# Optimization experiments

Hardware: AMD Instinct MI355X
Metric: run time of the kernel (lower is better)

Reference implementation:

```python
import jax, jax.numpy as jnp
import numpy as np

L, B, E, H, T, V = 256, 64, 256, 256, 16, 50000  # H = per-direction hidden; hidden_dim = 2H


def setup_inputs() -> dict:
    key = jax.random.key(0)
    ks = jax.random.split(key, 32)
    lengths = jnp.sort(jax.random.randint(ks[0], (B,), L // 2, L + 1))[::-1]  # descending, as pack_padded requires
    tokens = jax.random.randint(ks[1], (L, B), 1, V)
    valid = jnp.arange(L)[:, None] < lengths[None, :]
    tokens = jnp.where(valid, tokens, 0)  # pad_index = 0

    def gp(k, shape, s=0.1):
        return jax.random.normal(k, shape, dtype=jnp.float32) * s

    inp = {"tokens": tokens, "lengths": lengths, "emb": gp(ks[2], (V, E))}
    i = 3
    for layer, din in [(0, E), (1, 2 * H)]:
        for d in ("f", "b"):
            inp["w_ih_l%d%s" % (layer, d)] = gp(ks[i], (4 * H, din)); i += 1
            inp["w_hh_l%d%s" % (layer, d)] = gp(ks[i], (4 * H, H)); i += 1
            inp["b_ih_l%d%s" % (layer, d)] = gp(ks[i], (4 * H,)); i += 1
            inp["b_hh_l%d%s" % (layer, d)] = gp(ks[i], (4 * H,)); i += 1
    inp["w_out"] = gp(ks[i], (T, 2 * H)); i += 1
    inp["b_out"] = gp(ks[i], (T,)); i += 1
    inp["start_trans"] = gp(ks[i], (T,)); i += 1
    inp["end_trans"] = gp(ks[i], (T,)); i += 1
    inp["trans"] = gp(ks[i], (T, T))
    return inp


def lstm_layer(x, w_ih, w_hh, b_ih, b_hh):
    # x: [L, B, Din]; PyTorch gate order i, f, g, o; zero init state
    Hd = w_hh.shape[1]
    h0 = jnp.zeros((x.shape[1], Hd), x.dtype)

    def step(carry, xt):
        h, c = carry
        g = xt @ w_ih.T + b_ih + h @ w_hh.T + b_hh
        i, f, gg, o = jnp.split(g, 4, axis=-1)
        c = jax.nn.sigmoid(f) * c + jax.nn.sigmoid(i) * jnp.tanh(gg)
        h = jax.nn.sigmoid(o) * jnp.tanh(c)
        return (h, c), h

    _, ys = jax.lax.scan(step, (h0, h0), x)
    return ys  # [L, B, H]


def reverse_padded(x, lengths):
    # per-sequence time reversal over the first `length` steps (packed-sequence semantics)
    Ls = x.shape[0]
    t = jnp.arange(Ls)[:, None]
    idx = jnp.where(t < lengths[None, :], lengths[None, :] - 1 - t, t)  # [L, B]
    return jnp.take_along_axis(x, idx[:, :, None], axis=0)


def viterbi(emissions, mask, start_trans, end_trans, trans):
    # emissions [L, B, T], mask [L, B] bool -- pytorch-crf Viterbi decode, vectorized over batch
    score0 = start_trans[None, :] + emissions[0]  # [B, T]

    def step(score, inp):
        em_t, m_t = inp  # [B, T], [B]
        nxt = score[:, :, None] + trans[None, :, :] + em_t[:, None, :]  # [B, T, T]
        best = nxt.max(axis=1)
        idx = nxt.argmax(axis=1)  # index of previous tag
        score = jnp.where(m_t[:, None], best, score)  # freeze past end-of-sequence
        return score, idx

    score, hist = jax.lax.scan(step, score0, (emissions[1:], mask[1:]))  # hist [L-1, B, T]
    score = score + end_trans[None, :]
    best_score = score.max(axis=-1)
    last_tag = score.argmax(axis=-1)  # [B]

    def back(cur, inp):
        h_t, m_t = inp
        prev = jnp.take_along_axis(h_t, cur[:, None], axis=1)[:, 0]
        cur = jnp.where(m_t, prev, cur)
        return cur, cur

    _, tags_head = jax.lax.scan(back, last_tag, (hist, mask[1:]), reverse=True)  # [L-1, B]
    tags = jnp.concatenate([tags_head, last_tag[None, :]], axis=0)  # [L, B]
    tags = jnp.where(mask, tags, 0)
    return best_score, tags.astype(jnp.int32)


def reference(tokens, lengths, emb,
              w_ih_l0f, w_hh_l0f, b_ih_l0f, b_hh_l0f,
              w_ih_l0b, w_hh_l0b, b_ih_l0b, b_hh_l0b,
              w_ih_l1f, w_hh_l1f, b_ih_l1f, b_hh_l1f,
              w_ih_l1b, w_hh_l1b, b_ih_l1b, b_hh_l1b,
              w_out, b_out, start_trans, end_trans, trans):
    mask = tokens != 0  # pad_index = 0
    x = emb[tokens]  # [L, B, E]
    layers = [((w_ih_l0f, w_hh_l0f, b_ih_l0f, b_hh_l0f), (w_ih_l0b, w_hh_l0b, b_ih_l0b, b_hh_l0b)),
              ((w_ih_l1f, w_hh_l1f, b_ih_l1f, b_hh_l1f), (w_ih_l1b, w_hh_l1b, b_ih_l1b, b_hh_l1b))]
    for pf, pb in layers:
        fwd = lstm_layer(x, *pf)
        bwd = reverse_padded(lstm_layer(reverse_padded(x, lengths), *pb), lengths)
        x = jnp.concatenate([fwd, bwd], axis=-1) * mask[:, :, None]  # zero pads like pad_packed_sequence
    emissions = x @ w_out.T + b_out  # [L, B, T]
    best_score, tags = viterbi(emissions, mask, start_trans, end_trans, trans)
    return best_score, tags
```

## Files before the change

### kernel.cpp

```cpp
#include <hip/hip_runtime.h>
#include <hip/hip_bf16.h>
#include <math.h>

#define LSEQ 256
#define BB   64
#define EE   256
#define HH   256

__global__ __launch_bounds__(64)
void embed_kernel(const int* __restrict__ tokens, const float* __restrict__ emb,
                  float* __restrict__ x0) {
    int r = blockIdx.x;
    int tok = tokens[r];
    const float4* src = (const float4*)(emb + (size_t)tok * EE);
    float4* dst = (float4*)(x0 + (size_t)r * EE);
    dst[threadIdx.x] = src[threadIdx.x];
}

__global__ __launch_bounds__(256)
void pack_w3_kernel(const float* __restrict__ w0, const float* __restrict__ w1,
                    const float* __restrict__ w2, const float* __restrict__ w3,
                    float* __restrict__ W3) {
    __shared__ float t[16][65];
    const float* w = blockIdx.z == 0 ? w0 : blockIdx.z == 1 ? w1 : blockIdx.z == 2 ? w2 : w3;
    float* out = W3 + (size_t)blockIdx.z * 262144;
    int ut = blockIdx.y;
    int g = blockIdx.x >> 2, kt = blockIdx.x & 3;
    int k0 = kt * 64, tid = threadIdx.x;
    for (int e = tid; e < 1024; e += 256) {
        int ul = e >> 6, kl = e & 63;
        t[ul][kl] = w[(size_t)(g * 256 + ut * 16 + ul) * 256 + k0 + kl];
    }
    __syncthreads();
    for (int e = tid; e < 1024; e += 256) {
        int kl = e >> 4, ul = e & 15;
        out[(size_t)(ut * 256 + k0 + kl) * 64 + g * 16 + ul] = t[ul][kl];
    }
}

__global__ __launch_bounds__(256)
void init_cnt_kernel(int* __restrict__ cnt) {
    cnt[blockIdx.x * 256 + threadIdx.x] = 0;
}

__global__ __launch_bounds__(256)
void gemm_bias_kernel(const float* __restrict__ A, const float* __restrict__ W,
                      const float* __restrict__ b1, const float* __restrict__ b2,
                      float* __restrict__ C, int M, int N, int K) {
    const int BK = 16;
    __shared__ float As[BK][128];
    __shared__ float Bs[BK][128];
    int tid = threadIdx.x;
    int bm = blockIdx.x * 128;
    int bn = blockIdx.y * 128;
    int tm = (tid >> 4) << 3;
    int tn = (tid & 15) << 3;
    int lr = tid >> 1;
    int lc = (tid & 1) << 3;
    const float* Ap = A + (size_t)(bm + lr) * K + lc;
    const float* Wpt = W + (size_t)(bn + lr) * K + lc;
    float acc[8][8];
#pragma unroll
    for (int i = 0; i < 8; i++)
#pragma unroll
        for (int j = 0; j < 8; j++) acc[i][j] = 0.f;

    for (int k0 = 0; k0 < K; k0 += BK) {
        float4 a0 = *(const float4*)(Ap + k0);
        float4 a1 = *(const float4*)(Ap + k0 + 4);
        float4 w0 = *(const float4*)(Wpt + k0);
        float4 w1 = *(const float4*)(Wpt + k0 + 4);
        __syncthreads();
        As[lc+0][lr]=a0.x; As[lc+1][lr]=a0.y; As[lc+2][lr]=a0.z; As[lc+3][lr]=a0.w;
        As[lc+4][lr]=a1.x; As[lc+5][lr]=a1.y; As[lc+6][lr]=a1.z; As[lc+7][lr]=a1.w;
        Bs[lc+0][lr]=w0.x; Bs[lc+1][lr]=w0.y; Bs[lc+2][lr]=w0.z; Bs[lc+3][lr]=w0.w;
        Bs[lc+4][lr]=w1.x; Bs[lc+5][lr]=w1.y; Bs[lc+6][lr]=w1.z; Bs[lc+7][lr]=w1.w;
        __syncthreads();
#pragma unroll
        for (int k = 0; k < BK; k++) {
            float av[8], bv[8];
            *(float4*)&av[0] = *(const float4*)&As[k][tm];
            *(float4*)&av[4] = *(const float4*)&As[k][tm+4];
            *(float4*)&bv[0] = *(const float4*)&Bs[k][tn];
            *(float4*)&bv[4] = *(const float4*)&Bs[k][tn+4];
#pragma unroll
            for (int i = 0; i < 8; i++)
#pragma unroll
                for (int j = 0; j < 8; j++) acc[i][j] = fmaf(av[i], bv[j], acc[i][j]);
        }
    }
    float bj[8];
#pragma unroll
    for (int j = 0; j < 8; j++) bj[j] = b1[bn+tn+j] + b2[bn+tn+j];
#pragma unroll
    for (int i = 0; i < 8; i++) {
        float4 v0, v1;
        v0.x = acc[i][0]+bj[0]; v0.y = acc[i][1]+bj[1]; v0.z = acc[i][2]+bj[2]; v0.w = acc[i][3]+bj[3];
        v1.x = acc[i][4]+bj[4]; v1.y = acc[i][5]+bj[5]; v1.z = acc[i][6]+bj[6]; v1.w = acc[i][7]+bj[7];
        *(float4*)&C[(size_t)(bm+tm+i)*N + bn+tn]     = v0;
        *(float4*)&C[(size_t)(bm+tm+i)*N + bn+tn + 4] = v1;
    }
}

__global__ __launch_bounds__(256, 1)
void lstm_scan_kernel(const float* __restrict__ Gf, const float* __restrict__ Gb,
                      const float* __restrict__ W3f, const float* __restrict__ W3b,
                      const int* __restrict__ lengths, float* __restrict__ xout,
                      float* __restrict__ hg, int* __restrict__ cnt) {
    const int bid = blockIdx.x;
    const int dom = bid & 15;
    const int ut  = bid >> 4;
    const int dir = dom & 1;
    const int bt  = dom >> 1;
    const float* __restrict__ G = dir ? Gb : Gf;
    const float* __restrict__ W3 = (dir ? W3b : W3f) + (size_t)ut * 16384;
    float* hgD = hg + (size_t)dom * 4096;
    int* cntD = cnt + (size_t)dom * 8192;

    __shared__ float hs[2048];
    __shared__ float P[4096];
    __shared__ float lds_pad[16384];

    const int tid = threadIdx.x;
    const int kg = tid >> 5;
    const int cw = tid & 31;
    const int cb = (tid >> 4) & 7;
    const int cu = tid & 15;
    const int bg = bt * 8 + cb;
    const int ug = ut * 16 + cu;
    const int mylen = lengths[bg];

    float2 wreg[32];
#pragma unroll
    for (int kk = 0; kk < 32; kk++)
        wreg[kk] = *(const float2*)&W3[(size_t)(kg * 32 + kk) * 64 + cw * 2];

#pragma unroll
    for (int i = 0; i < 2; i++)
        *(float4*)&hs[(tid + 256 * i) * 4] = make_float4(0.f, 0.f, 0.f, 0.f);
    if (tid == 0 && mylen < 0) lds_pad[0] = 1.f;

    float cstate = 0.f;
    int tcur = dir ? (mylen - 1) : 0;
    const float* gr0 = G + ((size_t)tcur * BB + bg) * 1024 + ug;
    float gp0 = gr0[0], gp1 = gr0[256], gp2 = gr0[512], gp3 = gr0[768];
    __syncthreads();

    for (int s = 0; s < LSEQ; s++) {
        if (s > 0) {
            if (tid == 0) {
                const int* cp = &cntD[(s - 1) * 32];
                while (__hip_atomic_load(cp, __ATOMIC_RELAXED, __HIP_MEMORY_SCOPE_AGENT) < 16)
                    __builtin_amdgcn_s_sleep(1);
            }
            __syncthreads();
            const unsigned long long* src =
                (const unsigned long long*)(hgD + ((s - 1) & 1) * 2048);
            unsigned long long v[4];
#pragma unroll
            for (int i = 0; i < 4; i++)
                v[i] = __hip_atomic_load(src + tid + 256 * i, __ATOMIC_RELAXED,
                                         __HIP_MEMORY_SCOPE_AGENT);
#pragma unroll
            for (int i = 0; i < 4; i++)
                *(unsigned long long*)&hs[(tid + 256 * i) * 2] = v[i];
            __syncthreads();
        }

        float2 acc[8];
        const float4* h4 = (const float4*)hs;
#pragma unroll
        for (int b = 0; b < 8; b++) {
            float2 a = make_float2(0.f, 0.f);
            int hbase = b * 64 + kg * 8;
#pragma unroll
            for (int q = 0; q < 8; q++) {
                float4 hv = h4[hbase + q];
                a.x = fmaf(wreg[q*4+0].x, hv.x, a.x); a.y = fmaf(wreg[q*4+0].y, hv.x, a.y);
                a.x = fmaf(wreg[q*4+1].x, hv.y, a.x); a.y = fmaf(wreg[q*4+1].y, hv.y, a.y);
                a.x = fmaf(wreg[q*4+2].x, hv.z, a.x); a.y = fmaf(wreg[q*4+2].y, hv.z, a.y);
                a.x = fmaf(wreg[q*4+3].x, hv.w, a.x); a.y = fmaf(wreg[q*4+3].y, hv.w, a.y);
            }
            acc[b] = a;
        }
        const int wofs = (cw * 2) ^ (kg * 2);
#pragma unroll
        for (int b = 0; b < 8; b++)
            *(float2*)&P[kg * 512 + b * 64 + wofs] = acc[b];
        __syncthreads();

        float h = 0.f;
        if (tid < 128) {
            float g0 = gp0, g1 = gp1, g2 = gp2, g3 = gp3;
#pragma unroll
            for (int k2 = 0; k2 < 8; k2++) {
                int base = k2 * 512 + cb * 64;
                int x = k2 * 2;
                g0 += P[base + ((cu)      ^ x)];
                g1 += P[base + ((16 + cu) ^ x)];
                g2 += P[base + ((32 + cu) ^ x)];
                g3 += P[base + ((48 + cu) ^ x)];
            }
            float iv = 1.f / (1.f + expf(-g0));
            float fv = 1.f / (1.f + expf(-g1));
            float gv = tanhf(g2);
            float ov = 1.f / (1.f + expf(-g3));
            cstate = fv * cstate + iv * gv;
            h = ov * tanhf(cstate);
            atomicExch(&hgD[(s & 1) * 2048 + cb * 256 + ug], h);
        }
        asm volatile("s_waitcnt vmcnt(0)" ::: "memory");
        __syncthreads();
        if (tid == 0) atomicAdd(&cntD[s * 32], 1);

        if (tid < 128) {
            xout[(size_t)(tcur * BB + bg) * 512 + dir * 256 + ug] = (s < mylen) ? h : 0.f;
            if (s < 255) {
                int s2 = s + 1;
                tcur = dir ? (s2 < mylen ? mylen - 1 - s2 : s2) : s2;
                const float* gr = G + ((size_t)tcur * BB + bg) * 1024 + ug;
                gp0 = gr[0]; gp1 = gr[256]; gp2 = gr[512]; gp3 = gr[768];
            }
        }
    }
}

__global__ __launch_bounds__(256)
void emis_kernel(const float* __restrict__ x, const float* __restrict__ w_out,
                 const float* __restrict__ b_out, float* __restrict__ em) {
    __shared__ float ws_[16][516];
    __shared__ float xs[16][516];
    int tid = threadIdx.x;
    size_t r0 = (size_t)blockIdx.x * 16;
    for (int i4 = tid; i4 < 2048; i4 += 256) {
        int r = i4 >> 7, k4 = (i4 & 127) << 2;
        *(float4*)&ws_[r][k4] = *(const float4*)&w_out[r*512 + k4];
        *(float4*)&xs[r][k4]  = *(const float4*)&x[(r0 + r)*512 + k4];
    }
    __syncthreads();
    int rr = tid >> 4, n = tid & 15;
    const float4* xr = (const float4*)&xs[rr][0];
    const float4* wr = (const float4*)&ws_[n][0];
    float4 s; s.x = s.y = s.z = s.w = 0.f;
#pragma unroll 8
    for (int k = 0; k < 128; k++) {
        float4 a = xr[k], b = wr[k];
        s.x = fmaf(a.x,b.x,s.x); s.y = fmaf(a.y,b.y,s.y);
        s.z = fmaf(a.z,b.z,s.z); s.w = fmaf(a.w,b.w,s.w);
    }
    em[(r0+rr)*16 + n] = s.x+s.y+s.z+s.w + b_out[n];
}

__global__ __launch_bounds__(64)
void viterbi_kernel(const float* __restrict__ em, const int* __restrict__ tokens,
                    const float* __restrict__ start_trans, const float* __restrict__ end_trans,
                    const float* __restrict__ trans, float* __restrict__ out) {
    __shared__ float em_s[256][16];
    __shared__ float tr_s[16][16];
    __shared__ float sc[16];
    __shared__ unsigned char hist[255][16];
    int b = blockIdx.x, tid = threadIdx.x;
    for (int i = tid; i < 4096; i += 64) {
        int t = i >> 4, n = i & 15;
        em_s[t][n] = em[(size_t)t*1024 + b*16 + n];
    }
    for (int i = tid; i < 256; i += 64) ((float*)tr_s)[i] = trans[i];
    __syncthreads();
    if (tid < 16) sc[tid] = start_trans[tid] + em_s[0][tid];
    __syncthreads();
    for (int t = 1; t < 256; t++) {
        float best = 0.f; int arg = 0;
        if (tid < 16) {
            best = sc[0] + tr_s[0][tid];
#pragma unroll
            for (int i = 1; i < 16; i++) {
                float v = sc[i] + tr_s[i][tid];
                if (v > best) { best = v; arg = i; }
            }
            best += em_s[t][tid];
            hist[t-1][tid] = (unsigned char)arg;
        }
        bool m = tokens[t*64 + b] != 0;
        __syncthreads();
        if (tid < 16 && m) sc[tid] = best;
        __syncthreads();
    }
    if (tid == 0) {
        float best = sc[0] + end_trans[0]; int cur = 0;
        for (int jj = 1; jj < 16; jj++) {
            float v = sc[jj] + end_trans[jj];
            if (v > best) { best = v; cur = jj; }
        }
        out[b] = best;
        float* tags = out + 64;
        tags[255*64 + b] = (tokens[255*64+b] != 0) ? (float)cur : 0.f;
        for (int t = 254; t >= 0; t--) {
            if (tokens[(t+1)*64 + b] != 0) cur = hist[t][cur];
            tags[t*64 + b] = (tokens[t*64+b] != 0) ? (float)cur : 0.f;
        }
    }
}

extern "C" void kernel_launch(void* const* d_in, const int* in_sizes, int n_in,
                              void* d_out, int out_size, void* d_ws, size_t ws_size,
                              hipStream_t stream) {
    const int*   tokens   = (const int*)d_in[0];
    const int*   lengths  = (const int*)d_in[1];
    const float* emb      = (const float*)d_in[2];
    const float* w_ih_l0f = (const float*)d_in[3];
    const float* w_hh_l0f = (const float*)d_in[4];
    const float* b_ih_l0f = (const float*)d_in[5];
    const float* b_hh_l0f = (const float*)d_in[6];
    const float* w_ih_l0b = (const float*)d_in[7];
    const float* w_hh_l0b = (const float*)d_in[8];
    const float* b_ih_l0b = (const float*)d_in[9];
    const float* b_hh_l0b = (const float*)d_in[10];
    const float* w_ih_l1f = (const float*)d_in[11];
    const float* w_hh_l1f = (const float*)d_in[12];
    const float* b_ih_l1f = (const float*)d_in[13];
    const float* b_hh_l1f = (const float*)d_in[14];
    const float* w_ih_l1b = (const float*)d_in[15];
    const float* w_hh_l1b = (const float*)d_in[16];
    const float* b_ih_l1b = (const float*)d_in[17];
    const float* b_hh_l1b = (const float*)d_in[18];
    const float* w_out    = (const float*)d_in[19];
    const float* b_out    = (const float*)d_in[20];
    const float* start_tr = (const float*)d_in[21];
    const float* end_tr   = (const float*)d_in[22];
    const float* trans    = (const float*)d_in[23];

    float* ws  = (float*)d_ws;
    float* x0  = ws;
    float* x1  = x0 + 4194304;
    float* x2  = x1 + 8388608;
    float* Gf  = x2 + 8388608;
    float* Gb  = Gf + 16777216;
    float* W3  = Gb + 16777216;
    float* W3l0f = W3, *W3l0b = W3 + 262144, *W3l1f = W3 + 524288, *W3l1b = W3 + 786432;
    float* em  = x0;
    float* hg  = x0 + 1048576;
    int*   cnt = (int*)(x0 + 1179648);

    embed_kernel<<<16384, 64, 0, stream>>>(tokens, emb, x0);
    pack_w3_kernel<<<dim3(16, 16, 4), 256, 0, stream>>>(w_hh_l0f, w_hh_l0b, w_hh_l1f, w_hh_l1b, W3);

    dim3 gg(128, 8);
    gemm_bias_kernel<<<gg, 256, 0, stream>>>(x0, w_ih_l0f, b_ih_l0f, b_hh_l0f, Gf, 16384, 1024, 256);
    gemm_bias_kernel<<<gg, 256, 0, stream>>>(x0, w_ih_l0b, b_ih_l0b, b_hh_l0b, Gb, 16384, 1024, 256);
    init_cnt_kernel<<<1024, 256, 0, stream>>>(cnt);
    lstm_scan_kernel<<<256, 256, 0, stream>>>(Gf, Gb, W3l0f, W3l0b, lengths, x1, hg, cnt);

    gemm_bias_kernel<<<gg, 256, 0, stream>>>(x1, w_ih_l1f, b_ih_l1f, b_hh_l1f, Gf, 16384, 1024, 512);
    gemm_bias_kernel<<<gg, 256, 0, stream>>>(x1, w_ih_l1b, b_ih_l1b, b_hh_l1b, Gb, 16384, 1024, 512);
    lstm_scan_kernel<<<256, 256, 0, stream>>>(Gf, Gb, W3l1f, W3l1b, lengths, x2, hg, cnt + 131072);

    emis_kernel<<<1024, 256, 0, stream>>>(x2, w_out, b_out, em);
    viterbi_kernel<<<64, 64, 0, stream>>>(em, tokens, start_tr, end_tr, trans, (float*)d_out);
}
```

Measured before the change: 2.365 ms.

## Replace counter barrier with step-tagged hidden-state words in LSTM scan

Each hidden value is now published as a 64-bit word: the float in the low half and a step tag in the high half. Consumers spin directly on these words until every tag matches the expected step. This removes the per-step counter atomic, the single-thread spin, the memory-wait fence and one block barrier from the serial recurrence. It also drops the counter-reset kernel. In exchange the hidden-state buffer doubles in size, each thread polls eight words instead of reading four, and correctness now depends on stale tags in the reused workspace never matching the expected values.

```diff
diff --git a/kernel.cpp b/kernel.cpp
--- a/kernel.cpp
+++ b/kernel.cpp
@@ -36,11 +36,6 @@
         int kl = e >> 4, ul = e & 15;
         out[(size_t)(ut * 256 + k0 + kl) * 64 + g * 16 + ul] = t[ul][kl];
     }
-}
-
-__global__ __launch_bounds__(256)
-void init_cnt_kernel(int* __restrict__ cnt) {
-    cnt[blockIdx.x * 256 + threadIdx.x] = 0;
 }
 
 __global__ __launch_bounds__(256)
@@ -106,7 +101,7 @@
 void lstm_scan_kernel(const float* __restrict__ Gf, const float* __restrict__ Gb,
                       const float* __restrict__ W3f, const float* __restrict__ W3b,
                       const int* __restrict__ lengths, float* __restrict__ xout,
-                      float* __restrict__ hg, int* __restrict__ cnt) {
+                      unsigned long long* __restrict__ hg, int tagbase) {
     const int bid = blockIdx.x;
     const int dom = bid & 15;
     const int ut  = bid >> 4;
@@ -114,8 +109,7 @@
     const int bt  = dom >> 1;
     const float* __restrict__ G = dir ? Gb : Gf;
     const float* __restrict__ W3 = (dir ? W3b : W3f) + (size_t)ut * 16384;
-    float* hgD = hg + (size_t)dom * 4096;
-    int* cntD = cnt + (size_t)dom * 8192;
+    unsigned long long* hgD = hg + (size_t)dom * 4096;
 
     __shared__ float hs[2048];
     __shared__ float P[4096];
@@ -148,22 +142,27 @@
 
     for (int s = 0; s < LSEQ; s++) {
         if (s > 0) {
-            if (tid == 0) {
-                const int* cp = &cntD[(s - 1) * 32];
-                while (__hip_atomic_load(cp, __ATOMIC_RELAXED, __HIP_MEMORY_SCOPE_AGENT) < 16)
-                    __builtin_amdgcn_s_sleep(1);
-            }
-            __syncthreads();
-            const unsigned long long* src =
-                (const unsigned long long*)(hgD + ((s - 1) & 1) * 2048);
-            unsigned long long v[4];
-#pragma unroll
-            for (int i = 0; i < 4; i++)
+            const unsigned exp = (unsigned)(tagbase + s - 1);
+            const unsigned long long* src = hgD + ((s - 1) & 1) * 2048;
+            unsigned long long v[8];
+#pragma unroll
+            for (int i = 0; i < 8; i++)
                 v[i] = __hip_atomic_load(src + tid + 256 * i, __ATOMIC_RELAXED,
                                          __HIP_MEMORY_SCOPE_AGENT);
-#pragma unroll
-            for (int i = 0; i < 4; i++)
-                *(unsigned long long*)&hs[(tid + 256 * i) * 2] = v[i];
+            for (;;) {
+                bool ok = true;
+#pragma unroll
+                for (int i = 0; i < 8; i++) ok &= ((unsigned)(v[i] >> 32) == exp);
+                if (ok) break;
+#pragma unroll
+                for (int i = 0; i < 8; i++)
+                    if ((unsigned)(v[i] >> 32) != exp)
+                        v[i] = __hip_atomic_load(src + tid + 256 * i, __ATOMIC_RELAXED,
+                                                 __HIP_MEMORY_SCOPE_AGENT);
+            }
+#pragma unroll
+            for (int i = 0; i < 8; i++)
+                hs[tid + 256 * i] = __uint_as_float((unsigned)v[i]);
             __syncthreads();
         }
 
@@ -189,7 +188,6 @@
             *(float2*)&P[kg * 512 + b * 64 + wofs] = acc[b];
         __syncthreads();
 
-        float h = 0.f;
         if (tid < 128) {
             float g0 = gp0, g1 = gp1, g2 = gp2, g3 = gp3;
 #pragma unroll
@@ -206,14 +204,10 @@
             float gv = tanhf(g2);
             float ov = 1.f / (1.f + expf(-g3));
             cstate = fv * cstate + iv * gv;
-            h = ov * tanhf(cstate);
-            atomicExch(&hgD[(s & 1) * 2048 + cb * 256 + ug], h);
-        }
-        asm volatile("s_waitcnt vmcnt(0)" ::: "memory");
-        __syncthreads();
-        if (tid == 0) atomicAdd(&cntD[s * 32], 1);
-
-        if (tid < 128) {
+            float h = ov * tanhf(cstate);
+            unsigned long long pv =
+                ((unsigned long long)(unsigned)(tagbase + s) << 32) | __float_as_uint(h);
+            atomicExch(&hgD[(s & 1) * 2048 + cb * 256 + ug], pv);
             xout[(size_t)(tcur * BB + bg) * 512 + dir * 256 + ug] = (s < mylen) ? h : 0.f;
             if (s < 255) {
                 int s2 = s + 1;
@@ -338,8 +332,7 @@
     float* W3  = Gb + 16777216;
     float* W3l0f = W3, *W3l0b = W3 + 262144, *W3l1f = W3 + 524288, *W3l1b = W3 + 786432;
     float* em  = x0;
-    float* hg  = x0 + 1048576;
-    int*   cnt = (int*)(x0 + 1179648);
+    unsigned long long* hg = (unsigned long long*)(x0 + 1048576);
 
     embed_kernel<<<16384, 64, 0, stream>>>(tokens, emb, x0);
     pack_w3_kernel<<<dim3(16, 16, 4), 256, 0, stream>>>(w_hh_l0f, w_hh_l0b, w_hh_l1f, w_hh_l1b, W3);
@@ -347,12 +340,11 @@
     dim3 gg(128, 8);
     gemm_bias_kernel<<<gg, 256, 0, stream>>>(x0, w_ih_l0f, b_ih_l0f, b_hh_l0f, Gf, 16384, 1024, 256);
     gemm_bias_kernel<<<gg, 256, 0, stream>>>(x0, w_ih_l0b, b_ih_l0b, b_hh_l0b, Gb, 16384, 1024, 256);
-    init_cnt_kernel<<<1024, 256, 0, stream>>>(cnt);
-    lstm_scan_kernel<<<256, 256, 0, stream>>>(Gf, Gb, W3l0f, W3l0b, lengths, x1, hg, cnt);
+    lstm_scan_kernel<<<256, 256, 0, stream>>>(Gf, Gb, W3l0f, W3l0b, lengths, x1, hg, 1);
 
     gemm_bias_kernel<<<gg, 256, 0, stream>>>(x1, w_ih_l1f, b_ih_l1f, b_hh_l1f, Gf, 16384, 1024, 512);
     gemm_bias_kernel<<<gg, 256, 0, stream>>>(x1, w_ih_l1b, b_ih_l1b, b_hh_l1b, Gb, 16384, 1024, 512);
-    lstm_scan_kernel<<<256, 256, 0, stream>>>(Gf, Gb, W3l1f, W3l1b, lengths, x2, hg, cnt + 131072);
+    lstm_scan_kernel<<<256, 256, 0, stream>>>(Gf, Gb, W3l1f, W3l1b, lengths, x2, hg, 257);
 
     emis_kernel<<<1024, 256, 0, stream>>>(x2, w_out, b_out, em);
     viterbi_kernel<<<64, 64, 0, stream>>>(em, tokens, start_tr, end_tr, trans, (float*)d_out);
```

Result: slower. 2.676 ms (+13.1%).

## Replace per-step counter barrier with per-block flags and per-wave waits

Applied to the files above, without the earlier changes.

Replaces the shared atomic counter in the persistent LSTM scan with per-producer monotonic flags. Each wave now polls only the four producer blocks whose hidden-state slice it needs, which removes the block-wide barriers around the h exchange. The h layout is changed so each producer writes a contiguous chunk using paired 64-bit atomic stores, and the lds_pad occupancy limiter is dropped. This shortens the inter-block dependency chain on each timestep, at the cost of trickier memory-ordering correctness (it relies on compiler fences only, with no block barrier before the matvec).

```diff
diff --git a/kernel.cpp b/kernel.cpp
--- a/kernel.cpp
+++ b/kernel.cpp
@@ -5,7 +5,6 @@
 #define LSEQ 256
 #define BB   64
 #define EE   256
-#define HH   256
 
 __global__ __launch_bounds__(64)
 void embed_kernel(const int* __restrict__ tokens, const float* __restrict__ emb,
@@ -39,8 +38,8 @@
 }
 
 __global__ __launch_bounds__(256)
-void init_cnt_kernel(int* __restrict__ cnt) {
-    cnt[blockIdx.x * 256 + threadIdx.x] = 0;
+void init_flags_kernel(int* __restrict__ flags) {
+    flags[blockIdx.x * 256 + threadIdx.x] = 0;
 }
 
 __global__ __launch_bounds__(256)
@@ -106,7 +105,7 @@
 void lstm_scan_kernel(const float* __restrict__ Gf, const float* __restrict__ Gb,
                       const float* __restrict__ W3f, const float* __restrict__ W3b,
                       const int* __restrict__ lengths, float* __restrict__ xout,
-                      float* __restrict__ hg, int* __restrict__ cnt) {
+                      float* __restrict__ hg, int* __restrict__ flags) {
     const int bid = blockIdx.x;
     const int dom = bid & 15;
     const int ut  = bid >> 4;
@@ -115,17 +114,15 @@
     const float* __restrict__ G = dir ? Gb : Gf;
     const float* __restrict__ W3 = (dir ? W3b : W3f) + (size_t)ut * 16384;
     float* hgD = hg + (size_t)dom * 4096;
-    int* cntD = cnt + (size_t)dom * 8192;
+    int* flgD  = flags + dom * 512;
 
     __shared__ float hs[2048];
     __shared__ float P[4096];
-    __shared__ float lds_pad[16384];
 
     const int tid = threadIdx.x;
-    const int kg = tid >> 5;
-    const int cw = tid & 31;
-    const int cb = (tid >> 4) & 7;
-    const int cu = tid & 15;
+    const int kg = tid >> 5, cw = tid & 31;
+    const int w  = tid >> 6, lane = tid & 63;
+    const int cb = (tid >> 4) & 7, cu = tid & 15;
     const int bg = bt * 8 + cb;
     const int ug = ut * 16 + cu;
     const int mylen = lengths[bg];
@@ -136,35 +133,39 @@
         wreg[kk] = *(const float2*)&W3[(size_t)(kg * 32 + kk) * 64 + cw * 2];
 
 #pragma unroll
-    for (int i = 0; i < 2; i++)
-        *(float4*)&hs[(tid + 256 * i) * 4] = make_float4(0.f, 0.f, 0.f, 0.f);
-    if (tid == 0 && mylen < 0) lds_pad[0] = 1.f;
+    for (int i = 0; i < 8; i++) hs[tid + 256 * i] = 0.f;
 
     float cstate = 0.f;
     int tcur = dir ? (mylen - 1) : 0;
-    const float* gr0 = G + ((size_t)tcur * BB + bg) * 1024 + ug;
-    float gp0 = gr0[0], gp1 = gr0[256], gp2 = gr0[512], gp3 = gr0[768];
+    float gp0 = 0.f, gp1 = 0.f, gp2 = 0.f, gp3 = 0.f;
+    if (tid < 128) {
+        const float* gr = G + ((size_t)(tcur * BB + bg)) * 1024 + ug;
+        gp0 = gr[0]; gp1 = gr[256]; gp2 = gr[512]; gp3 = gr[768];
+    }
     __syncthreads();
 
     for (int s = 0; s < LSEQ; s++) {
         if (s > 0) {
-            if (tid == 0) {
-                const int* cp = &cntD[(s - 1) * 32];
-                while (__hip_atomic_load(cp, __ATOMIC_RELAXED, __HIP_MEMORY_SCOPE_AGENT) < 16)
+            if (lane < 4) {
+                const int* fp = &flgD[(4 * w + lane) * 32];
+                while (__hip_atomic_load(fp, __ATOMIC_RELAXED, __HIP_MEMORY_SCOPE_AGENT) < s)
                     __builtin_amdgcn_s_sleep(1);
             }
-            __syncthreads();
+            asm volatile("" ::: "memory");
             const unsigned long long* src =
-                (const unsigned long long*)(hgD + ((s - 1) & 1) * 2048);
+                (const unsigned long long*)(hgD + ((s - 1) & 1) * 2048) + w * 256;
             unsigned long long v[4];
 #pragma unroll
             for (int i = 0; i < 4; i++)
-                v[i] = __hip_atomic_load(src + tid + 256 * i, __ATOMIC_RELAXED,
+                v[i] = __hip_atomic_load(src + lane + 64 * i, __ATOMIC_RELAXED,
                                          __HIP_MEMORY_SCOPE_AGENT);
 #pragma unroll
-            for (int i = 0; i < 4; i++)
-                *(unsigned long long*)&hs[(tid + 256 * i) * 2] = v[i];
-            __syncthreads();
+            for (int i = 0; i < 4; i++) {
+                int fo = 512 * w + 2 * (lane + 64 * i);
+                hs[fo]     = __uint_as_float((unsigned)v[i]);
+                hs[fo + 1] = __uint_as_float((unsigned)(v[i] >> 32));
+            }
+            asm volatile("" ::: "memory");
         }
 
         float2 acc[8];
@@ -172,14 +173,24 @@
 #pragma unroll
         for (int b = 0; b < 8; b++) {
             float2 a = make_float2(0.f, 0.f);
-            int hbase = b * 64 + kg * 8;
-#pragma unroll
-            for (int q = 0; q < 8; q++) {
-                float4 hv = h4[hbase + q];
-                a.x = fmaf(wreg[q*4+0].x, hv.x, a.x); a.y = fmaf(wreg[q*4+0].y, hv.x, a.y);
-                a.x = fmaf(wreg[q*4+1].x, hv.y, a.x); a.y = fmaf(wreg[q*4+1].y, hv.y, a.y);
-                a.x = fmaf(wreg[q*4+2].x, hv.z, a.x); a.y = fmaf(wreg[q*4+2].y, hv.z, a.y);
-                a.x = fmaf(wreg[q*4+3].x, hv.w, a.x); a.y = fmaf(wreg[q*4+3].y, hv.w, a.y);
+            int hb0 = 64 * kg + 4 * b;
+#pragma unroll
+            for (int q = 0; q < 4; q++) {
+                float4 hv = h4[hb0 + q];
+                float2 w0 = wreg[q*4+0], w1 = wreg[q*4+1], w2 = wreg[q*4+2], w3v = wreg[q*4+3];
+                a.x = fmaf(w0.x, hv.x, a.x); a.y = fmaf(w0.y, hv.x, a.y);
+                a.x = fmaf(w1.x, hv.y, a.x); a.y = fmaf(w1.y, hv.y, a.y);
+                a.x = fmaf(w2.x, hv.z, a.x); a.y = fmaf(w2.y, hv.z, a.y);
+                a.x = fmaf(w3v.x, hv.w, a.x); a.y = fmaf(w3v.y, hv.w, a.y);
+            }
+#pragma unroll
+            for (int q = 0; q < 4; q++) {
+                float4 hv = h4[hb0 + 32 + q];
+                float2 w0 = wreg[16+q*4+0], w1 = wreg[16+q*4+1], w2 = wreg[16+q*4+2], w3v = wreg[16+q*4+3];
+                a.x = fmaf(w0.x, hv.x, a.x); a.y = fmaf(w0.y, hv.x, a.y);
+                a.x = fmaf(w1.x, hv.y, a.x); a.y = fmaf(w1.y, hv.y, a.y);
+                a.x = fmaf(w2.x, hv.z, a.x); a.y = fmaf(w2.y, hv.z, a.y);
+                a.x = fmaf(w3v.x, hv.w, a.x); a.y = fmaf(w3v.y, hv.w, a.y);
             }
             acc[b] = a;
         }
@@ -191,34 +202,37 @@
 
         float h = 0.f;
         if (tid < 128) {
-            float g0 = gp0, g1 = gp1, g2 = gp2, g3 = gp3;
+            float a0 = gp0, a1 = gp1, a2 = gp2, a3 = gp3;
 #pragma unroll
             for (int k2 = 0; k2 < 8; k2++) {
-                int base = k2 * 512 + cb * 64;
-                int x = k2 * 2;
-                g0 += P[base + ((cu)      ^ x)];
-                g1 += P[base + ((16 + cu) ^ x)];
-                g2 += P[base + ((32 + cu) ^ x)];
-                g3 += P[base + ((48 + cu) ^ x)];
-            }
-            float iv = 1.f / (1.f + expf(-g0));
-            float fv = 1.f / (1.f + expf(-g1));
-            float gv = tanhf(g2);
-            float ov = 1.f / (1.f + expf(-g3));
+                int base = k2 * 512 + cb * 64, x = k2 * 2;
+                a0 += P[base + ((cu)      ^ x)];
+                a1 += P[base + ((16 + cu) ^ x)];
+                a2 += P[base + ((32 + cu) ^ x)];
+                a3 += P[base + ((48 + cu) ^ x)];
+            }
+            float iv = 1.f / (1.f + expf(-a0));
+            float fv = 1.f / (1.f + expf(-a1));
+            float gv = tanhf(a2);
+            float ov = 1.f / (1.f + expf(-a3));
             cstate = fv * cstate + iv * gv;
             h = ov * tanhf(cstate);
-            atomicExch(&hgD[(s & 1) * 2048 + cb * 256 + ug], h);
+            float hp = __shfl_xor(h, 1);
+            if (!(cu & 1)) {
+                unsigned long long pv =
+                    ((unsigned long long)__float_as_uint(hp) << 32) | __float_as_uint(h);
+                atomicExch((unsigned long long*)&hgD[(s & 1) * 2048 + ut * 128 + cb * 16 + cu], pv);
+            }
         }
         asm volatile("s_waitcnt vmcnt(0)" ::: "memory");
         __syncthreads();
-        if (tid == 0) atomicAdd(&cntD[s * 32], 1);
-
+        if (tid == 0) atomicExch(&flgD[ut * 32], s + 1);
         if (tid < 128) {
             xout[(size_t)(tcur * BB + bg) * 512 + dir * 256 + ug] = (s < mylen) ? h : 0.f;
-            if (s < 255) {
+            if (s < LSEQ - 1) {
                 int s2 = s + 1;
                 tcur = dir ? (s2 < mylen ? mylen - 1 - s2 : s2) : s2;
-                const float* gr = G + ((size_t)tcur * BB + bg) * 1024 + ug;
+                const float* gr = G + ((size_t)(tcur * BB + bg)) * 1024 + ug;
                 gp0 = gr[0]; gp1 = gr[256]; gp2 = gr[512]; gp3 = gr[768];
             }
         }
@@ -339,7 +353,7 @@
     float* W3l0f = W3, *W3l0b = W3 + 262144, *W3l1f = W3 + 524288, *W3l1b = W3 + 786432;
     float* em  = x0;
     float* hg  = x0 + 1048576;
-    int*   cnt = (int*)(x0 + 1179648);
+    int*   flags = (int*)(x0 + 1114112);
 
     embed_kernel<<<16384, 64, 0, stream>>>(tokens, emb, x0);
     pack_w3_kernel<<<dim3(16, 16, 4), 256, 0, stream>>>(w_hh_l0f, w_hh_l0b, w_hh_l1f, w_hh_l1b, W3);
@@ -347,12 +361,12 @@
     dim3 gg(128, 8);
     gemm_bias_kernel<<<gg, 256, 0, stream>>>(x0, w_ih_l0f, b_ih_l0f, b_hh_l0f, Gf, 16384, 1024, 256);
     gemm_bias_kernel<<<gg, 256, 0, stream>>>(x0, w_ih_l0b, b_ih_l0b, b_hh_l0b, Gb, 16384, 1024, 256);
-    init_cnt_kernel<<<1024, 256, 0, stream>>>(cnt);
-    lstm_scan_kernel<<<256, 256, 0, stream>>>(Gf, Gb, W3l0f, W3l0b, lengths, x1, hg, cnt);
+    init_flags_kernel<<<64, 256, 0, stream>>>(flags);
+    lstm_scan_kernel<<<256, 256, 0, stream>>>(Gf, Gb, W3l0f, W3l0b, lengths, x1, hg, flags);
 
     gemm_bias_kernel<<<gg, 256, 0, stream>>>(x1, w_ih_l1f, b_ih_l1f, b_hh_l1f, Gf, 16384, 1024, 512);
     gemm_bias_kernel<<<gg, 256, 0, stream>>>(x1, w_ih_l1b, b_ih_l1b, b_hh_l1b, Gb, 16384, 1024, 512);
-    lstm_scan_kernel<<<256, 256, 0, stream>>>(Gf, Gb, W3l1f, W3l1b, lengths, x2, hg, cnt + 131072);
+    lstm_scan_kernel<<<256, 256, 0, stream>>>(Gf, Gb, W3l1f, W3l1b, lengths, x2, hg, flags + 8192);
 
     emis_kernel<<<1024, 256, 0, stream>>>(x2, w_out, b_out, em);
     viterbi_kernel<<<64, 64, 0, stream>>>(em, tokens, start_tr, end_tr, trans, (float*)d_out);
```

Measured after the change: 2.513 ms. +6.3%, slower.
